# Kernel tuning notes

Hardware: AMD Instinct MI355X
Metric: run time of the kernel (lower is better)

## Reference

```python
import jax, jax.numpy as jnp
import numpy as np

HID = 32
NUM_GRAPHS = 256
N_NODES = 100000


def graph_conv(x, src, dst, ew, rel_w, rel_b, root_w):
    # PyG GraphConv: out = lin_rel(sum_{j in N(i)} e_ji * x_j) + lin_root(x_i)
    msg = x[src] * ew[:, None]                                  # [E, F] gather
    agg = jax.ops.segment_sum(msg, dst, num_segments=N_NODES)    # [N, F] scatter-add
    return agg @ rel_w + rel_b + x @ root_w


def setup_inputs() -> dict:
    key = jax.random.key(0)
    ks = jax.random.split(key, 16)
    N, E, F = N_NODES, 1600000, 64
    x = jax.random.normal(ks[0], (N, F), dtype=jnp.float32)
    edge_index = jax.random.randint(ks[1], (2, E), 0, N, dtype=jnp.int64)
    edge_attr = jax.random.uniform(ks[2], (E,), dtype=jnp.float32)
    batch = jnp.sort(jax.random.randint(ks[3], (N,), 0, NUM_GRAPHS, dtype=jnp.int64))
    s = lambda k, shp: jax.random.normal(k, shp, dtype=jnp.float32) * 0.1
    return {
        "x": x, "edge_index": edge_index, "edge_attr": edge_attr, "batch": batch,
        "conv1_rel_w": s(ks[4], (F, HID)), "conv1_rel_b": jnp.zeros((HID,), jnp.float32),
        "conv1_root_w": s(ks[5], (F, HID)),
        "conv2_rel_w": s(ks[6], (HID, HID)), "conv2_rel_b": jnp.zeros((HID,), jnp.float32),
        "conv2_root_w": s(ks[7], (HID, HID)),
        "lin1_w": s(ks[8], (HID, 32)), "lin1_b": jnp.zeros((32,), jnp.float32),
        "lin2_w": s(ks[9], (32, 16)), "lin2_b": jnp.zeros((16,), jnp.float32),
        "lin_w": s(ks[10], (16, 1)), "lin_b": jnp.zeros((1,), jnp.float32),
    }


def reference(x, edge_index, edge_attr, batch,
              conv1_rel_w, conv1_rel_b, conv1_root_w,
              conv2_rel_w, conv2_rel_b, conv2_root_w,
              lin1_w, lin1_b, lin2_w, lin2_b, lin_w, lin_b):
    src, dst = edge_index[0], edge_index[1]
    h = jax.nn.relu(graph_conv(x, src, dst, edge_attr, conv1_rel_w, conv1_rel_b, conv1_root_w))
    h = jax.nn.relu(graph_conv(h, src, dst, edge_attr, conv2_rel_w, conv2_rel_b, conv2_root_w))
    # global mean pool over graphs
    sums = jax.ops.segment_sum(h, batch, num_segments=NUM_GRAPHS)          # [G, 32]
    cnts = jax.ops.segment_sum(jnp.ones((h.shape[0],), h.dtype), batch, num_segments=NUM_GRAPHS)
    g = sums / jnp.maximum(cnts, 1.0)[:, None]
    # dropout is identity in eval mode
    g = jax.nn.relu(g @ lin1_w + lin1_b)
    g = g @ lin2_w + lin2_b
    g = jax.nn.relu(g)
    return g @ lin_w + lin_b  # [G, 1]
```

## Files before the change

kernel.cpp:

```cpp
#include <hip/hip_runtime.h>
#include <hip/hip_fp16.h>

#define NGRAPH 256
#define FIN 64
#define HID 32
#define NB_SHIFT 8
#define NB_NODES 256
#define KMAX2 512
#define EPB 2048
#define EPT 8
#define NT 64
#define XPAD 65
#define HPAD 33
#define PCAP 6016

union SU {
    int h[KMAX2];
    struct { float Wr[FIN * HID]; float Wo[FIN * HID]; float b[HID];
             float x[NT * XPAD]; } g;
};

__global__ __launch_bounds__(256, 4) void hist_lin64(
    const int* __restrict__ dst, int* __restrict__ cbb, int E, int K, int NBLK,
    const float* __restrict__ x, const float* __restrict__ Wrel,
    const float* __restrict__ Wroot, const float* __restrict__ bias,
    __half* __restrict__ A, float* __restrict__ B, int N)
{
    __shared__ SU u;
    int tid = threadIdx.x;
    if (blockIdx.x < (unsigned)NBLK) {
        for (int i = tid; i < K; i += 256) u.h[i] = 0;
        __syncthreads();
        int e0 = blockIdx.x * EPB + tid * 8;
        if (e0 + 7 < E) {
            int4 d0 = *reinterpret_cast<const int4*>(dst + e0);
            int4 d1 = *reinterpret_cast<const int4*>(dst + e0 + 4);
            atomicAdd(&u.h[d0.x >> NB_SHIFT], 1); atomicAdd(&u.h[d0.y >> NB_SHIFT], 1);
            atomicAdd(&u.h[d0.z >> NB_SHIFT], 1); atomicAdd(&u.h[d0.w >> NB_SHIFT], 1);
            atomicAdd(&u.h[d1.x >> NB_SHIFT], 1); atomicAdd(&u.h[d1.y >> NB_SHIFT], 1);
            atomicAdd(&u.h[d1.z >> NB_SHIFT], 1); atomicAdd(&u.h[d1.w >> NB_SHIFT], 1);
        } else {
            for (int e = e0; e < E && e < e0 + 8; ++e)
                atomicAdd(&u.h[dst[e] >> NB_SHIFT], 1);
        }
        __syncthreads();
        for (int i = tid; i < K; i += 256)
            cbb[(size_t)i * NBLK + blockIdx.x] = u.h[i];
        return;
    }
    {
        const float4* Wr4 = (const float4*)Wrel;
        const float4* Wo4 = (const float4*)Wroot;
        for (int i = tid; i < FIN * HID / 4; i += 256) {
            ((float4*)u.g.Wr)[i] = Wr4[i];
            ((float4*)u.g.Wo)[i] = Wo4[i];
        }
        if (tid < HID) u.g.b[tid] = bias[tid];
    }
    int base = (blockIdx.x - NBLK) * NT;
    {
        const float4* x4 = (const float4*)x;
        for (int i = tid; i < NT * 16; i += 256) {
            int row = i >> 4, c4 = i & 15;
            int n = base + row;
            float4 v = (n < N) ? x4[(size_t)n * 16 + c4]
                               : make_float4(0.f, 0.f, 0.f, 0.f);
            *(float4*)&u.g.x[row * XPAD + c4 * 4] = v;
        }
    }
    __syncthreads();

    int nl = tid >> 3;
    int fq = (tid & 7) * 4;
    const float* xa = &u.g.x[nl * XPAD];
    const float* xb = &u.g.x[(nl + 32) * XPAD];
    float4 ar0 = make_float4(0.f,0.f,0.f,0.f), ao0 = ar0;
    float4 ar1 = ar0, ao1 = ar0;
    #pragma unroll 4
    for (int k = 0; k < FIN; ++k) {
        float4 w4 = *(const float4*)&u.g.Wr[k * HID + fq];
        float4 o4 = *(const float4*)&u.g.Wo[k * HID + fq];
        float va = xa[k], vb = xb[k];
        ar0.x = fmaf(va, w4.x, ar0.x); ar0.y = fmaf(va, w4.y, ar0.y);
        ar0.z = fmaf(va, w4.z, ar0.z); ar0.w = fmaf(va, w4.w, ar0.w);
        ao0.x = fmaf(va, o4.x, ao0.x); ao0.y = fmaf(va, o4.y, ao0.y);
        ao0.z = fmaf(va, o4.z, ao0.z); ao0.w = fmaf(va, o4.w, ao0.w);
        ar1.x = fmaf(vb, w4.x, ar1.x); ar1.y = fmaf(vb, w4.y, ar1.y);
        ar1.z = fmaf(vb, w4.z, ar1.z); ar1.w = fmaf(vb, w4.w, ar1.w);
        ao1.x = fmaf(vb, o4.x, ao1.x); ao1.y = fmaf(vb, o4.y, ao1.y);
        ao1.z = fmaf(vb, o4.z, ao1.z); ao1.w = fmaf(vb, o4.w, ao1.w);
    }
    float4 bb = *(const float4*)&u.g.b[fq];
    int n0 = base + nl, n1 = base + nl + 32;
    if (n0 < N) {
        __half2 pa = __floats2half2_rn(ar0.x, ar0.y);
        __half2 pb = __floats2half2_rn(ar0.z, ar0.w);
        uint2 pk; pk.x = *(unsigned*)&pa; pk.y = *(unsigned*)&pb;
        *(uint2*)&A[(size_t)n0 * HID + fq] = pk;
        ao0.x += bb.x; ao0.y += bb.y; ao0.z += bb.z; ao0.w += bb.w;
        *(float4*)&B[(size_t)n0 * HID + fq] = ao0;
    }
    if (n1 < N) {
        __half2 pa = __floats2half2_rn(ar1.x, ar1.y);
        __half2 pb = __floats2half2_rn(ar1.z, ar1.w);
        uint2 pk; pk.x = *(unsigned*)&pa; pk.y = *(unsigned*)&pb;
        *(uint2*)&A[(size_t)n1 * HID + fq] = pk;
        ao1.x += bb.x; ao1.y += bb.y; ao1.z += bb.z; ao1.w += bb.w;
        *(float4*)&B[(size_t)n1 * HID + fq] = ao1;
    }
}

__global__ __launch_bounds__(256, 4) void node_lin32(
    const float* __restrict__ Hpre, const float* __restrict__ Wrel,
    const float* __restrict__ Wroot, const float* __restrict__ bias,
    __half* __restrict__ A, float* __restrict__ C, int N)
{
    __shared__ float sWr[HID * HID];
    __shared__ float sWo[HID * HID];
    __shared__ float sb[HID];
    __shared__ float sh[NT * HPAD];
    int tid = threadIdx.x;
    {
        const float4* Wr4 = (const float4*)Wrel;
        const float4* Wo4 = (const float4*)Wroot;
        for (int i = tid; i < HID * HID / 4; i += 256) {
            ((float4*)sWr)[i] = Wr4[i];
            ((float4*)sWo)[i] = Wo4[i];
        }
        if (tid < HID) sb[tid] = bias[tid];
    }
    int base = blockIdx.x * NT;
    {
        const float4* H4 = (const float4*)Hpre;
        for (int i = tid; i < NT * 8; i += 256) {
            int row = i >> 3, c4 = i & 7;
            int n = base + row;
            float4 v = make_float4(0.f, 0.f, 0.f, 0.f);
            if (n < N) {
                v = H4[(size_t)n * 8 + c4];
                v.x = v.x > 0.f ? v.x : 0.f; v.y = v.y > 0.f ? v.y : 0.f;
                v.z = v.z > 0.f ? v.z : 0.f; v.w = v.w > 0.f ? v.w : 0.f;
            }
            *(float4*)&sh[row * HPAD + c4 * 4] = v;
        }
    }
    __syncthreads();

    int nl = tid >> 3;
    int fq = (tid & 7) * 4;
    const float* xa = &sh[nl * HPAD];
    const float* xb = &sh[(nl + 32) * HPAD];
    float4 ar0 = make_float4(0.f,0.f,0.f,0.f), ao0 = ar0;
    float4 ar1 = ar0, ao1 = ar0;
    #pragma unroll 4
    for (int k = 0; k < HID; ++k) {
        float4 w4 = *(const float4*)&sWr[k * HID + fq];
        float4 o4 = *(const float4*)&sWo[k * HID + fq];
        float va = xa[k], vb = xb[k];
        ar0.x = fmaf(va, w4.x, ar0.x); ar0.y = fmaf(va, w4.y, ar0.y);
        ar0.z = fmaf(va, w4.z, ar0.z); ar0.w = fmaf(va, w4.w, ar0.w);
        ao0.x = fmaf(va, o4.x, ao0.x); ao0.y = fmaf(va, o4.y, ao0.y);
        ao0.z = fmaf(va, o4.z, ao0.z); ao0.w = fmaf(va, o4.w, ao0.w);
        ar1.x = fmaf(vb, w4.x, ar1.x); ar1.y = fmaf(vb, w4.y, ar1.y);
        ar1.z = fmaf(vb, w4.z, ar1.z); ar1.w = fmaf(vb, w4.w, ar1.w);
        ao1.x = fmaf(vb, o4.x, ao1.x); ao1.y = fmaf(vb, o4.y, ao1.y);
        ao1.z = fmaf(vb, o4.z, ao1.z); ao1.w = fmaf(vb, o4.w, ao1.w);
    }
    float4 bb = *(const float4*)&sb[fq];
    int n0 = base + nl, n1 = base + nl + 32;
    if (n0 < N) {
        __half2 pa = __floats2half2_rn(ar0.x, ar0.y);
        __half2 pb = __floats2half2_rn(ar0.z, ar0.w);
        uint2 pk; pk.x = *(unsigned*)&pa; pk.y = *(unsigned*)&pb;
        *(uint2*)&A[(size_t)n0 * HID + fq] = pk;
        ao0.x += bb.x; ao0.y += bb.y; ao0.z += bb.z; ao0.w += bb.w;
        *(float4*)&C[(size_t)n0 * HID + fq] = ao0;
    }
    if (n1 < N) {
        __half2 pa = __floats2half2_rn(ar1.x, ar1.y);
        __half2 pb = __floats2half2_rn(ar1.z, ar1.w);
        uint2 pk; pk.x = *(unsigned*)&pa; pk.y = *(unsigned*)&pb;
        *(uint2*)&A[(size_t)n1 * HID + fq] = pk;
        ao1.x += bb.x; ao1.y += bb.y; ao1.z += bb.z; ao1.w += bb.w;
        *(float4*)&C[(size_t)n1 * HID + fq] = ao1;
    }
}


__global__ __launch_bounds__(256) void bucket_scan(
    int* __restrict__ cbb, int* __restrict__ btot, int NBLK)
{
    __shared__ int sc[256];
    size_t row = (size_t)blockIdx.x * NBLK;
    int t = threadIdx.x;
    int base = t * 4;
    int v[4]; int s = 0;
    #pragma unroll
    for (int j = 0; j < 4; ++j) { v[j] = (base + j < NBLK) ? cbb[row + base + j] : 0; s += v[j]; }
    sc[t] = s;
    __syncthreads();
    int acc = s;
    for (int off = 1; off < 256; off <<= 1) {
        int add = (t >= off) ? sc[t - off] : 0;
        __syncthreads();
        acc += add;
        sc[t] = acc;
        __syncthreads();
    }
    int run = acc - s;
    #pragma unroll
    for (int j = 0; j < 4; ++j) {
        if (base + j < NBLK) cbb[row + base + j] = run;
        run += v[j];
    }
    if (t == 255) btot[blockIdx.x] = acc;
}

__global__ __launch_bounds__(256) void btot_scan(
    const int* __restrict__ btot, int* __restrict__ bbase, int K)
{
    __shared__ int sc[256];
    int t = threadIdx.x;
    int base = t * 4;
    int v[4]; int s = 0;
    #pragma unroll
    for (int j = 0; j < 4; ++j) { v[j] = (base + j < K) ? btot[base + j] : 0; s += v[j]; }
    sc[t] = s;
    __syncthreads();
    int acc = s;
    for (int off = 1; off < 256; off <<= 1) {
        int add = (t >= off) ? sc[t - off] : 0;
        __syncthreads();
        acc += add;
        sc[t] = acc;
        __syncthreads();
    }
    int run = acc - s;
    #pragma unroll
    for (int j = 0; j < 4; ++j) {
        if (base + j < K) bbase[base + j] = run;
        run += v[j];
    }
    if (t == 255) bbase[K] = acc;
}

__global__ __launch_bounds__(256) void partB(
    const int* __restrict__ src, const int* __restrict__ dst,
    const float* __restrict__ ew, const int* __restrict__ cbb,
    const int* __restrict__ bbase, int2* __restrict__ stg8,
    int E, int K, int NBLK)
{
    __shared__ int4 pay[EPB];
    __shared__ int h[KMAX2];
    __shared__ int lofs[KMAX2];
    __shared__ int gb[KMAX2];
    __shared__ int sc[256];
    int tid = threadIdx.x;
    for (int i = tid; i < K; i += 256) h[i] = 0;
    __syncthreads();

    int base = blockIdx.x * EPB;
    int es[EPT], ds[EPT]; float wsr[EPT];
    #pragma unroll
    for (int k = 0; k < EPT; ++k) {
        int e = base + k * 256 + tid;
        if (e < E) {
            es[k] = src[e]; ds[k] = dst[e]; wsr[k] = ew[e];
            atomicAdd(&h[ds[k] >> NB_SHIFT], 1);
        } else ds[k] = -1;
    }
    __syncthreads();

    int b0 = tid * 2;
    int v0 = (b0 < K) ? h[b0] : 0;
    int v1 = (b0 + 1 < K) ? h[b0 + 1] : 0;
    int s = v0 + v1;
    sc[tid] = s;
    __syncthreads();
    int acc = s;
    for (int off = 1; off < 256; off <<= 1) {
        int add = (tid >= off) ? sc[tid - off] : 0;
        __syncthreads();
        acc += add;
        sc[tid] = acc;
        __syncthreads();
    }
    int run = acc - s;
    if (b0 < K) lofs[b0] = run;
    if (b0 + 1 < K) lofs[b0 + 1] = run + v0;
    __syncthreads();

    for (int b = tid; b < K; b += 256) {
        gb[b] = bbase[b] + cbb[(size_t)b * NBLK + blockIdx.x];
        h[b] = lofs[b];
    }
    __syncthreads();

    #pragma unroll
    for (int k = 0; k < EPT; ++k) {
        if (ds[k] >= 0) {
            int b = ds[k] >> NB_SHIFT;
            int dloc = ds[k] & (NB_NODES - 1);
            int slot = atomicAdd(&h[b], 1);
            pay[slot] = make_int4(es[k] | (dloc << 17), __float_as_int(wsr[k]),
                                  gb[b] + slot - lofs[b], 0);
        }
    }
    __syncthreads();

    int tot = E - base; if (tot > EPB) tot = EPB;
    for (int i = tid; i < tot; i += 256) {
        int4 p = pay[i];
        stg8[p.z] = make_int2(p.x, p.y);
    }
}

__global__ __launch_bounds__(512) void partC2(
    const int2* __restrict__ stg8, const int* __restrict__ bbase,
    int* __restrict__ rowptr, int2* __restrict__ perm, int N, int K)
{
    __shared__ int2 pe[PCAP];
    __shared__ int hcnt[NB_NODES];
    __shared__ int hinc[NB_NODES];
    int b = blockIdx.x;
    int n0 = b << NB_SHIFT;
    int nTop = n0 + NB_NODES; if (nTop > N) nTop = N;
    int nloc = nTop - n0;
    int tid = threadIdx.x;
    if (tid < NB_NODES) hcnt[tid] = 0;
    int lo = bbase[b], hi = bbase[b + 1];
    int sz = hi - lo;
    bool fit = (sz <= PCAP);
    if (fit) {
        for (int i = tid; i < sz; i += 512) pe[i] = stg8[lo + i];
    }
    __syncthreads();
    if (fit) {
        for (int i = tid; i < sz; i += 512)
            atomicAdd(&hcnt[pe[i].x >> 17], 1);
    } else {
        for (int e = lo + tid; e < hi; e += 512)
            atomicAdd(&hcnt[stg8[e].x >> 17], 1);
    }
    __syncthreads();
    if (tid < NB_NODES) hinc[tid] = hcnt[tid];
    __syncthreads();
    for (int off = 1; off < NB_NODES; off <<= 1) {
        int v = (tid < NB_NODES && tid >= off) ? hinc[tid - off] : 0;
        __syncthreads();
        if (tid < NB_NODES) hinc[tid] += v;
        __syncthreads();
    }
    if (tid < nloc) {
        int excl = hinc[tid] - hcnt[tid];
        rowptr[n0 + tid] = lo + excl;
        hcnt[tid] = excl;
    }
    if (b == K - 1 && tid == 0) rowptr[N] = hi;
    __syncthreads();
    if (fit) {
        for (int i = tid; i < sz; i += 512) {
            int2 p = pe[i];
            int pos = lo + atomicAdd(&hcnt[p.x >> 17], 1);
            perm[pos] = make_int2(p.x & 0x1FFFF, p.y);
        }
    } else {
        for (int e = lo + tid; e < hi; e += 512) {
            int2 p = stg8[e];
            int pos = lo + atomicAdd(&hcnt[p.x >> 17], 1);
            perm[pos] = make_int2(p.x & 0x1FFFF, p.y);
        }
    }
}

__global__ __launch_bounds__(256) void csr_agg(
    const int* __restrict__ rowptr, const int2* __restrict__ perm,
    const __half* __restrict__ A, float* __restrict__ out, int N)
{
    int gid = blockIdx.x * 256 + threadIdx.x;
    int n = gid >> 3;
    if (n >= N) return;
    int q = threadIdx.x & 7;
    int e0 = rowptr[n], e1 = rowptr[n + 1];
    const uint2* A2 = (const uint2*)A;
    float4 a0 = make_float4(0.f, 0.f, 0.f, 0.f);
    float4 a1 = make_float4(0.f, 0.f, 0.f, 0.f);
    int e = e0;
    for (; e + 1 < e1; e += 2) {
        int2 p0 = perm[e];
        int2 p1 = perm[e + 1];
        uint2 r0 = A2[(size_t)p0.x * 8 + q];
        uint2 r1 = A2[(size_t)p1.x * 8 + q];
        float w0 = __int_as_float(p0.y), w1 = __int_as_float(p1.y);
        float2 f01 = __half22float2(*(__half2*)&r0.x);
        float2 f23 = __half22float2(*(__half2*)&r0.y);
        float2 g01 = __half22float2(*(__half2*)&r1.x);
        float2 g23 = __half22float2(*(__half2*)&r1.y);
        a0.x = fmaf(f01.x, w0, a0.x); a0.y = fmaf(f01.y, w0, a0.y);
        a0.z = fmaf(f23.x, w0, a0.z); a0.w = fmaf(f23.y, w0, a0.w);
        a1.x = fmaf(g01.x, w1, a1.x); a1.y = fmaf(g01.y, w1, a1.y);
        a1.z = fmaf(g23.x, w1, a1.z); a1.w = fmaf(g23.y, w1, a1.w);
    }
    if (e < e1) {
        int2 p = perm[e];
        uint2 r = A2[(size_t)p.x * 8 + q];
        float w = __int_as_float(p.y);
        float2 f01 = __half22float2(*(__half2*)&r.x);
        float2 f23 = __half22float2(*(__half2*)&r.y);
        a0.x = fmaf(f01.x, w, a0.x); a0.y = fmaf(f01.y, w, a0.y);
        a0.z = fmaf(f23.x, w, a0.z); a0.w = fmaf(f23.y, w, a0.w);
    }
    a0.x += a1.x; a0.y += a1.y; a0.z += a1.z; a0.w += a1.w;
    float4* O4 = (float4*)out;
    size_t oi = (size_t)n * 8 + q;
    float4 o = O4[oi];
    o.x += a0.x; o.y += a0.y; o.z += a0.z; o.w += a0.w;
    O4[oi] = o;
}

__global__ __launch_bounds__(256) void pool_mlp(
    const float* __restrict__ C, const int* __restrict__ batch, int N,
    const float* __restrict__ W1, const float* __restrict__ b1,
    const float* __restrict__ W2, const float* __restrict__ b2,
    const float* __restrict__ W3, const float* __restrict__ b3,
    float* __restrict__ out)
{
    int g = blockIdx.x;
    int tid = threadIdx.x;
    int lo, hi;
    {
        int l = 0, r = N;
        while (l < r) { int m = (l + r) >> 1; if (batch[m] < g) l = m + 1; else r = m; }
        lo = l;
        r = N;
        while (l < r) { int m = (l + r) >> 1; if (batch[m] < g + 1) l = m + 1; else r = m; }
        hi = l;
    }
    __shared__ float ssum[8][32];
    __shared__ float gvec[32];
    __shared__ float h1v[32];
    __shared__ float h2v[16];
    int f = tid & 31, seg = tid >> 5;
    float acc = 0.f;
    for (int n = lo + seg; n < hi; n += 8) {
        float v = C[(size_t)n * HID + f];
        acc += v > 0.f ? v : 0.f;
    }
    ssum[seg][f] = acc;
    __syncthreads();
    if (tid < 32) {
        float s = 0.f;
        #pragma unroll
        for (int k = 0; k < 8; ++k) s += ssum[k][tid];
        float c = (float)(hi - lo); c = c > 1.f ? c : 1.f;
        gvec[tid] = s / c;
    }
    __syncthreads();
    if (tid < 32) {
        float a = b1[tid];
        #pragma unroll
        for (int k = 0; k < 32; ++k) a = fmaf(gvec[k], W1[k * 32 + tid], a);
        h1v[tid] = a > 0.f ? a : 0.f;
    }
    __syncthreads();
    if (tid < 16) {
        float a = b2[tid];
        #pragma unroll
        for (int k = 0; k < 32; ++k) a = fmaf(h1v[k], W2[k * 16 + tid], a);
        h2v[tid] = a > 0.f ? a : 0.f;
    }
    __syncthreads();
    if (tid == 0) {
        float o = b3[0];
        #pragma unroll
        for (int k = 0; k < 16; ++k) o = fmaf(h2v[k], W3[k], o);
        out[g] = o;
    }
}

extern "C" void kernel_launch(void* const* d_in, const int* in_sizes, int n_in,
                              void* d_out, int out_size, void* d_ws, size_t ws_size,
                              hipStream_t stream) {
    const float* x     = (const float*)d_in[0];
    const int*   ei    = (const int*)d_in[1];
    const float* ew    = (const float*)d_in[2];
    const int*   batch = (const int*)d_in[3];
    const float* c1rw  = (const float*)d_in[4];
    const float* c1rb  = (const float*)d_in[5];
    const float* c1ow  = (const float*)d_in[6];
    const float* c2rw  = (const float*)d_in[7];
    const float* c2rb  = (const float*)d_in[8];
    const float* c2ow  = (const float*)d_in[9];
    const float* l1w   = (const float*)d_in[10];
    const float* l1b   = (const float*)d_in[11];
    const float* l2w   = (const float*)d_in[12];
    const float* l2b   = (const float*)d_in[13];
    const float* lw    = (const float*)d_in[14];
    const float* lb    = (const float*)d_in[15];

    int N = in_sizes[0] / FIN;
    int E = in_sizes[2];
    const int* src = ei;
    const int* dst = ei + E;
    int K    = (N + NB_NODES - 1) >> NB_SHIFT;
    int NBLK = (E + EPB - 1) / EPB;

    char* ws = (char*)d_ws;
    size_t off = 0;
    auto alloc = [&](size_t nbytes) { void* p = ws + off; off += (nbytes + 255) & ~size_t(255); return p; };
    __half* A     = (__half*)alloc((size_t)N * HID * 2);
    float*  BC    = (float*) alloc((size_t)N * HID * 4);
    int2*   perm  = (int2*)  alloc((size_t)E * 8);
    int2*   stg8  = (int2*)  alloc((size_t)E * 8);
    int*    cbb   = (int*)   alloc((size_t)K * NBLK * 4);
    int*   rowptr = (int*)   alloc((size_t)(N + 1) * 4);
    int*   btot   = (int*)   alloc((size_t)KMAX2 * 4);
    int*   bbase  = (int*)   alloc((size_t)(KMAX2 + 1) * 4);

    int nb_node = (N + NT - 1) / NT;
    int nb_agg  = (int)(((long long)N * 8 + 255) / 256);

    hist_lin64<<<NBLK + nb_node, 256, 0, stream>>>(
        dst, cbb, E, K, NBLK, x, c1rw, c1ow, c1rb, A, BC, N);
    bucket_scan<<<K, 256, 0, stream>>>(cbb, btot, NBLK);
    btot_scan<<<1, 256, 0, stream>>>(btot, bbase, K);
    partB<<<NBLK, 256, 0, stream>>>(src, dst, ew, cbb, bbase, stg8, E, K, NBLK);
    partC2<<<K, 512, 0, stream>>>(stg8, bbase, rowptr, perm, N, K);

    csr_agg<<<nb_agg, 256, 0, stream>>>(rowptr, perm, A, BC, N);
    node_lin32<<<nb_node, 256, 0, stream>>>(BC, c2rw, c2ow, c2rb, A, BC, N);
    csr_agg<<<nb_agg, 256, 0, stream>>>(rowptr, perm, A, BC, N);
    pool_mlp<<<NGRAPH, 256, 0, stream>>>(BC, batch, N, l1w, l1b, l2w, l2b, lw, lb,
                                         (float*)d_out);
}
```

Before: 160.9 us.

## Degree-sort nodes within buckets and unroll CSR aggregation by four

partC2 now counting-sorts each 256-node bucket's nodes by in-degree (capped at 63) and writes a node order array. csr_agg walks nodes in that order so neighbouring 8-lane groups in a wavefront have similar edge counts, which is meant to cut divergence from uneven loop trip counts. The aggregation loop is also unrolled from two to four edges with four accumulators to keep more gathers in flight. This costs an extra indirection load per node, scattered output rows, and a small serial scan in partC2.

```diff
diff --git a/kernel.cpp b/kernel.cpp
--- a/kernel.cpp
+++ b/kernel.cpp
@@ -317,17 +317,21 @@
 
 __global__ __launch_bounds__(512) void partC2(
     const int2* __restrict__ stg8, const int* __restrict__ bbase,
-    int* __restrict__ rowptr, int2* __restrict__ perm, int N, int K)
+    int* __restrict__ rowptr, int2* __restrict__ perm,
+    int* __restrict__ norder, int N, int K)
 {
     __shared__ int2 pe[PCAP];
     __shared__ int hcnt[NB_NODES];
     __shared__ int hinc[NB_NODES];
+    __shared__ int dh[64];
+    __shared__ int dof[64];
     int b = blockIdx.x;
     int n0 = b << NB_SHIFT;
     int nTop = n0 + NB_NODES; if (nTop > N) nTop = N;
     int nloc = nTop - n0;
     int tid = threadIdx.x;
     if (tid < NB_NODES) hcnt[tid] = 0;
+    if (tid >= NB_NODES && tid < NB_NODES + 64) dh[tid - NB_NODES] = 0;
     int lo = bbase[b], hi = bbase[b + 1];
     int sz = hi - lo;
     bool fit = (sz <= PCAP);
@@ -343,6 +347,7 @@
             atomicAdd(&hcnt[stg8[e].x >> 17], 1);
     }
     __syncthreads();
+    int deg = (tid < nloc) ? hcnt[tid] : -1;
     if (tid < NB_NODES) hinc[tid] = hcnt[tid];
     __syncthreads();
     for (int off = 1; off < NB_NODES; off <<= 1) {
@@ -371,37 +376,65 @@
             perm[pos] = make_int2(p.x & 0x1FFFF, p.y);
         }
     }
+    int dbin = (deg > 63) ? 63 : deg;
+    if (tid < nloc) atomicAdd(&dh[dbin], 1);
+    __syncthreads();
+    if (tid == 0) {
+        int run = 0;
+        #pragma unroll
+        for (int i = 0; i < 64; ++i) { dof[i] = run; run += dh[i]; dh[i] = 0; }
+    }
+    __syncthreads();
+    if (tid < nloc) {
+        int r = dof[dbin] + atomicAdd(&dh[dbin], 1);
+        norder[n0 + r] = n0 + tid;
+    }
 }
 
 __global__ __launch_bounds__(256) void csr_agg(
-    const int* __restrict__ rowptr, const int2* __restrict__ perm,
-    const __half* __restrict__ A, float* __restrict__ out, int N)
+    const int* __restrict__ rowptr, const int* __restrict__ norder,
+    const int2* __restrict__ perm, const __half* __restrict__ A,
+    float* __restrict__ out, int N)
 {
     int gid = blockIdx.x * 256 + threadIdx.x;
-    int n = gid >> 3;
-    if (n >= N) return;
+    int idx = gid >> 3;
+    if (idx >= N) return;
+    int n = norder[idx];
     int q = threadIdx.x & 7;
     int e0 = rowptr[n], e1 = rowptr[n + 1];
     const uint2* A2 = (const uint2*)A;
     float4 a0 = make_float4(0.f, 0.f, 0.f, 0.f);
-    float4 a1 = make_float4(0.f, 0.f, 0.f, 0.f);
+    float4 a1 = a0, a2 = a0, a3 = a0;
     int e = e0;
-    for (; e + 1 < e1; e += 2) {
+    for (; e + 3 < e1; e += 4) {
         int2 p0 = perm[e];
         int2 p1 = perm[e + 1];
+        int2 p2 = perm[e + 2];
+        int2 p3 = perm[e + 3];
         uint2 r0 = A2[(size_t)p0.x * 8 + q];
         uint2 r1 = A2[(size_t)p1.x * 8 + q];
+        uint2 r2 = A2[(size_t)p2.x * 8 + q];
+        uint2 r3 = A2[(size_t)p3.x * 8 + q];
         float w0 = __int_as_float(p0.y), w1 = __int_as_float(p1.y);
+        float w2 = __int_as_float(p2.y), w3 = __int_as_float(p3.y);
         float2 f01 = __half22float2(*(__half2*)&r0.x);
         float2 f23 = __half22float2(*(__half2*)&r0.y);
+        a0.x = fmaf(f01.x, w0, a0.x); a0.y = fmaf(f01.y, w0, a0.y);
+        a0.z = fmaf(f23.x, w0, a0.z); a0.w = fmaf(f23.y, w0, a0.w);
         float2 g01 = __half22float2(*(__half2*)&r1.x);
         float2 g23 = __half22float2(*(__half2*)&r1.y);
-        a0.x = fmaf(f01.x, w0, a0.x); a0.y = fmaf(f01.y, w0, a0.y);
-        a0.z = fmaf(f23.x, w0, a0.z); a0.w = fmaf(f23.y, w0, a0.w);
         a1.x = fmaf(g01.x, w1, a1.x); a1.y = fmaf(g01.y, w1, a1.y);
         a1.z = fmaf(g23.x, w1, a1.z); a1.w = fmaf(g23.y, w1, a1.w);
-    }
-    if (e < e1) {
+        float2 h01 = __half22float2(*(__half2*)&r2.x);
+        float2 h23 = __half22float2(*(__half2*)&r2.y);
+        a2.x = fmaf(h01.x, w2, a2.x); a2.y = fmaf(h01.y, w2, a2.y);
+        a2.z = fmaf(h23.x, w2, a2.z); a2.w = fmaf(h23.y, w2, a2.w);
+        float2 k01 = __half22float2(*(__half2*)&r3.x);
+        float2 k23 = __half22float2(*(__half2*)&r3.y);
+        a3.x = fmaf(k01.x, w3, a3.x); a3.y = fmaf(k01.y, w3, a3.y);
+        a3.z = fmaf(k23.x, w3, a3.z); a3.w = fmaf(k23.y, w3, a3.w);
+    }
+    for (; e < e1; ++e) {
         int2 p = perm[e];
         uint2 r = A2[(size_t)p.x * 8 + q];
         float w = __int_as_float(p.y);
@@ -410,7 +443,10 @@
         a0.x = fmaf(f01.x, w, a0.x); a0.y = fmaf(f01.y, w, a0.y);
         a0.z = fmaf(f23.x, w, a0.z); a0.w = fmaf(f23.y, w, a0.w);
     }
-    a0.x += a1.x; a0.y += a1.y; a0.z += a1.z; a0.w += a1.w;
+    a0.x += a1.x + a2.x + a3.x;
+    a0.y += a1.y + a2.y + a3.y;
+    a0.z += a1.z + a2.z + a3.z;
+    a0.w += a1.w + a2.w + a3.w;
     float4* O4 = (float4*)out;
     size_t oi = (size_t)n * 8 + q;
     float4 o = O4[oi];
@@ -508,14 +544,15 @@
     char* ws = (char*)d_ws;
     size_t off = 0;
     auto alloc = [&](size_t nbytes) { void* p = ws + off; off += (nbytes + 255) & ~size_t(255); return p; };
-    __half* A     = (__half*)alloc((size_t)N * HID * 2);
-    float*  BC    = (float*) alloc((size_t)N * HID * 4);
-    int2*   perm  = (int2*)  alloc((size_t)E * 8);
-    int2*   stg8  = (int2*)  alloc((size_t)E * 8);
-    int*    cbb   = (int*)   alloc((size_t)K * NBLK * 4);
-    int*   rowptr = (int*)   alloc((size_t)(N + 1) * 4);
-    int*   btot   = (int*)   alloc((size_t)KMAX2 * 4);
-    int*   bbase  = (int*)   alloc((size_t)(KMAX2 + 1) * 4);
+    __half* A      = (__half*)alloc((size_t)N * HID * 2);
+    float*  BC     = (float*) alloc((size_t)N * HID * 4);
+    int2*   perm   = (int2*)  alloc((size_t)E * 8);
+    int2*   stg8   = (int2*)  alloc((size_t)E * 8);
+    int*    cbb    = (int*)   alloc((size_t)K * NBLK * 4);
+    int*    rowptr = (int*)   alloc((size_t)(N + 1) * 4);
+    int*    norder = (int*)   alloc((size_t)N * 4);
+    int*    btot   = (int*)   alloc((size_t)KMAX2 * 4);
+    int*    bbase  = (int*)   alloc((size_t)(KMAX2 + 1) * 4);
 
     int nb_node = (N + NT - 1) / NT;
     int nb_agg  = (int)(((long long)N * 8 + 255) / 256);
@@ -525,11 +562,11 @@
     bucket_scan<<<K, 256, 0, stream>>>(cbb, btot, NBLK);
     btot_scan<<<1, 256, 0, stream>>>(btot, bbase, K);
     partB<<<NBLK, 256, 0, stream>>>(src, dst, ew, cbb, bbase, stg8, E, K, NBLK);
-    partC2<<<K, 512, 0, stream>>>(stg8, bbase, rowptr, perm, N, K);
-
-    csr_agg<<<nb_agg, 256, 0, stream>>>(rowptr, perm, A, BC, N);
+    partC2<<<K, 512, 0, stream>>>(stg8, bbase, rowptr, perm, norder, N, K);
+
+    csr_agg<<<nb_agg, 256, 0, stream>>>(rowptr, norder, perm, A, BC, N);
     node_lin32<<<nb_node, 256, 0, stream>>>(BC, c2rw, c2ow, c2rb, A, BC, N);
-    csr_agg<<<nb_agg, 256, 0, stream>>>(rowptr, perm, A, BC, N);
+    csr_agg<<<nb_agg, 256, 0, stream>>>(rowptr, norder, perm, A, BC, N);
     pool_mlp<<<NGRAPH, 256, 0, stream>>>(BC, batch, N, l1w, l1b, l2w, l2b, lw, lb,
                                          (float*)d_out);
 }
```

New measurement: 168.5 us. +4.7%, slower.
